# Performance work log

Measured on AMD Instinct MI355X. Metric: run time of the kernel, lower is better.

## Reference

```python
import jax, jax.numpy as jnp
import numpy as np

B, T, C, H = 256, 256, 384, 64  # batch, seq (= block_size), n_embd, head_size


def setup_inputs() -> dict:
    key = jax.random.key(0)
    kx, kq, kk, kv = jax.random.split(key, 4)
    x = jax.random.normal(kx, (B, T, C), dtype=jnp.float32)
    # nn.Linear(n_embd, head_size, bias=False) weights, stored transposed so y = x @ W
    scale = 1.0 / np.sqrt(C)
    Wq = jax.random.normal(kq, (C, H), dtype=jnp.float32) * scale
    Wk = jax.random.normal(kk, (C, H), dtype=jnp.float32) * scale
    Wv = jax.random.normal(kv, (C, H), dtype=jnp.float32) * scale
    return {"x": x, "Wq": Wq, "Wk": Wk, "Wv": Wv}


def reference(x, Wq, Wk, Wv):
    # Single causal self-attention head. NOTE: source scales by C**-0.5 where
    # C = n_embd (not head_size) — preserved faithfully. Dropout in eval mode
    # (identity) for a deterministic reference.
    Bv, Tv, Cv = x.shape
    q = x @ Wq                                   # [B, T, H]
    k = x @ Wk                                   # [B, T, H]
    v = x @ Wv                                   # [B, T, H]
    wei = jnp.einsum('bth,bsh->bts', q, k) * (Cv ** -0.5)  # [B, T, T]
    causal = jnp.tril(jnp.ones((Tv, Tv), dtype=bool))      # tril[:T,:T]
    wei = jnp.where(causal[None, :, :], wei, -jnp.inf)
    wei = jax.nn.softmax(wei, axis=-1)
    out = jnp.einsum('bts,bsh->bth', wei, v)     # [B, T, H]
    return out
```

## Files before the change

### kernel.cpp

```cpp
#include <hip/hip_runtime.h>
#include <hip/hip_bf16.h>

typedef __attribute__((ext_vector_type(8))) short bf16x8;
typedef __attribute__((ext_vector_type(4))) float f32x4;

__device__ __forceinline__ unsigned short f2bf(float f) {
    union { float f; unsigned int u; } v; v.f = f;
    unsigned int u = v.u;
    unsigned int r = u + 0x7FFFu + ((u >> 16) & 1u);
    return (unsigned short)(r >> 16);
}

__device__ __forceinline__ unsigned int cvtpk(float lo, float hi) {
    unsigned int r;
    asm("v_cvt_pk_bf16_f32 %0, %1, %2" : "=v"(r) : "v"(lo), "v"(hi));
    return r;
}

#define GLDS16(gsrc, ldst)                                                          \
    __builtin_amdgcn_global_load_lds(                                               \
        (const __attribute__((address_space(1))) unsigned int*)(gsrc),              \
        (__attribute__((address_space(3))) unsigned int*)(ldst), 16, 0, 0)

__global__ __launch_bounds__(256) void wprep(const float* __restrict__ Wq,
                                             const float* __restrict__ Wk,
                                             const float* __restrict__ Wv,
                                             unsigned short* __restrict__ Wt2) {
    int idx = blockIdx.x * 256 + threadIdx.x;
    if (idx >= 73728) return;
    int w   = idx / 24576;
    int rem = idx % 24576;
    int n = rem / 384, k = rem % 384;
    const float* W = (w == 0) ? Wq : ((w == 1) ? Wk : Wv);
    int col = w * 64 + n;
    Wt2[(size_t)(k >> 5) * 6144 + ((k >> 3) & 3) * 1536 + col * 8 + (k & 7)] = f2bf(W[k * 64 + n]);
}

#define QOFF  0
#define KOFF  36864
#define VTOFF 73728
#define POFF  107520

__global__ __launch_bounds__(512, 2) void fused(const float* __restrict__ x,
                                                const unsigned short* __restrict__ Wt2,
                                                float* __restrict__ out) {
    __shared__ __align__(16) char smem[147456];

    const int b = blockIdx.x;
    const int tid = threadIdx.x, lane = tid & 63, wid = tid >> 6;
    const int l15 = lane & 15, lg = lane >> 4;
    const float* xb = x + (size_t)b * 98304;
    float* ob = out + (size_t)b * 16384;

#pragma unroll
    for (int i = 0; i < 18; ++i) {
        int n = wid * 18 + i;
        GLDS16(Wt2 + (size_t)n * 512 + lane * 8, smem + n * 1024);
    }

    const float* xw = xb + (size_t)(wid * 32 + l15) * 384 + lg * 8;

    float4 p0[4], p1[4], p2[4];
#define XLOAD(P, C)                                                                 \
    P[0] = *reinterpret_cast<const float4*>(xw + (C) * 32);                         \
    P[1] = *reinterpret_cast<const float4*>(xw + (C) * 32 + 4);                     \
    P[2] = *reinterpret_cast<const float4*>(xw + 6144 + (C) * 32);                  \
    P[3] = *reinterpret_cast<const float4*>(xw + 6144 + (C) * 32 + 4);
    XLOAD(p0, 0)
    XLOAD(p1, 1)
    XLOAD(p2, 2)
    __builtin_amdgcn_sched_barrier(0);
    asm volatile("s_waitcnt vmcnt(12)" ::: "memory");
    __builtin_amdgcn_s_barrier();

    f32x4 acc[2][12] = {};

#define CHUNK(C, P, WAITN)                                                          \
    asm volatile("s_waitcnt vmcnt(" #WAITN ")" ::: "memory");                       \
    __builtin_amdgcn_sched_barrier(0);                                              \
    {                                                                               \
        union { unsigned int u[4]; bf16x8 v; } cv0, cv1;                            \
        cv0.u[0] = cvtpk(P[0].x, P[0].y); cv0.u[1] = cvtpk(P[0].z, P[0].w);         \
        cv0.u[2] = cvtpk(P[1].x, P[1].y); cv0.u[3] = cvtpk(P[1].z, P[1].w);         \
        cv1.u[0] = cvtpk(P[2].x, P[2].y); cv1.u[1] = cvtpk(P[2].z, P[2].w);         \
        cv1.u[2] = cvtpk(P[3].x, P[3].y); cv1.u[3] = cvtpk(P[3].z, P[3].w);         \
        bf16x8 a0 = cv0.v, a1 = cv1.v;                                              \
        if ((C) + 3 < 12) { XLOAD(P, (C) + 3) }                                     \
        __builtin_amdgcn_sched_barrier(0);                                          \
        const char* bs = smem + (C) * 12288 + lg * 3072 + l15 * 16;                 \
        _Pragma("unroll")                                                           \
        for (int n = 0; n < 12; ++n) {                                              \
            bf16x8 bf = *reinterpret_cast<const bf16x8*>(bs + n * 256);             \
            acc[0][n] = __builtin_amdgcn_mfma_f32_16x16x32_bf16(a0, bf, acc[0][n], 0, 0, 0); \
            acc[1][n] = __builtin_amdgcn_mfma_f32_16x16x32_bf16(a1, bf, acc[1][n], 0, 0, 0); \
        }                                                                           \
    }

    CHUNK(0,  p0, 8)
    CHUNK(1,  p1, 8)
    CHUNK(2,  p2, 8)
    CHUNK(3,  p0, 8)
    CHUNK(4,  p1, 8)
    CHUNK(5,  p2, 8)
    CHUNK(6,  p0, 8)
    CHUNK(7,  p1, 8)
    CHUNK(8,  p2, 8)
    CHUNK(9,  p0, 8)
    CHUNK(10, p1, 4)
    CHUNK(11, p2, 0)

    __syncthreads();

#pragma unroll
    for (int m = 0; m < 2; ++m) {
#pragma unroll
        for (int n = 0; n < 12; ++n) {
            int col = n * 16 + l15;
#pragma unroll
            for (int j = 0; j < 4; ++j) {
                int t = wid * 32 + m * 16 + lg * 4 + j;
                unsigned short hv = f2bf(acc[m][n][j]);
                if (col < 64)
                    *reinterpret_cast<unsigned short*>(smem + QOFF + (t * 72 + col) * 2) = hv;
                else if (col < 128)
                    *reinterpret_cast<unsigned short*>(smem + KOFF + (t * 72 + (col - 64)) * 2) = hv;
                else
                    *reinterpret_cast<unsigned short*>(smem + VTOFF + ((col - 128) * 264 + t) * 2) = hv;
            }
        }
    }
    __syncthreads();

    char* Pw = smem + POFF + wid * 4608;
    const int r0 = wid * 32;
    const float scale = 0.05103103630798287f;

    f32x4 o[2][4] = {};
    float M[2][4], L[2][4];
#pragma unroll
    for (int m = 0; m < 2; ++m)
#pragma unroll
        for (int j = 0; j < 4; ++j) { M[m][j] = -1e30f; L[m][j] = 0.f; }

    for (int jt = 0; jt <= (wid >> 1); ++jt) {
        f32x4 s[2][4] = {};
#pragma unroll
        for (int kk = 0; kk < 2; ++kk) {
            bf16x8 aq[2], bk[4];
#pragma unroll
            for (int m = 0; m < 2; ++m)
                aq[m] = *reinterpret_cast<const bf16x8*>(smem + QOFF + ((r0 + m * 16 + l15) * 72 + kk * 32 + lg * 8) * 2);
#pragma unroll
            for (int n = 0; n < 4; ++n)
                bk[n] = *reinterpret_cast<const bf16x8*>(smem + KOFF + ((jt * 64 + n * 16 + l15) * 72 + kk * 32 + lg * 8) * 2);
#pragma unroll
            for (int m = 0; m < 2; ++m)
#pragma unroll
                for (int n = 0; n < 4; ++n)
                    s[m][n] = __builtin_amdgcn_mfma_f32_16x16x32_bf16(aq[m], bk[n], s[m][n], 0, 0, 0);
        }
        float tm[2][4];
#pragma unroll
        for (int m = 0; m < 2; ++m)
#pragma unroll
            for (int j = 0; j < 4; ++j) tm[m][j] = -1e30f;
#pragma unroll
        for (int m = 0; m < 2; ++m) {
#pragma unroll
            for (int n = 0; n < 4; ++n) {
                int colg = jt * 64 + n * 16 + l15;
#pragma unroll
                for (int j = 0; j < 4; ++j) {
                    int rowg = r0 + m * 16 + lg * 4 + j;
                    float v = s[m][n][j] * scale;
                    if (colg > rowg) v = -1e30f;
                    s[m][n][j] = v;
                    tm[m][j] = fmaxf(tm[m][j], v);
                }
            }
        }
#pragma unroll
        for (int m = 0; m < 2; ++m)
#pragma unroll
            for (int j = 0; j < 4; ++j) {
                float v = tm[m][j];
                v = fmaxf(v, __shfl_xor(v, 1));
                v = fmaxf(v, __shfl_xor(v, 2));
                v = fmaxf(v, __shfl_xor(v, 4));
                v = fmaxf(v, __shfl_xor(v, 8));
                tm[m][j] = v;
            }
        float alpha[2][4];
#pragma unroll
        for (int m = 0; m < 2; ++m)
#pragma unroll
            for (int j = 0; j < 4; ++j) {
                float mn = fmaxf(M[m][j], tm[m][j]);
                alpha[m][j] = __expf(M[m][j] - mn);
                M[m][j] = mn;
            }
        float ts[2][4] = {};
#pragma unroll
        for (int m = 0; m < 2; ++m)
#pragma unroll
            for (int n = 0; n < 4; ++n)
#pragma unroll
                for (int j = 0; j < 4; ++j) {
                    float p = __expf(s[m][n][j] - M[m][j]);
                    s[m][n][j] = p;
                    ts[m][j] += p;
                }
#pragma unroll
        for (int m = 0; m < 2; ++m)
#pragma unroll
            for (int j = 0; j < 4; ++j) {
                float v = ts[m][j];
                v += __shfl_xor(v, 1);
                v += __shfl_xor(v, 2);
                v += __shfl_xor(v, 4);
                v += __shfl_xor(v, 8);
                L[m][j] = L[m][j] * alpha[m][j] + v;
            }
#pragma unroll
        for (int m = 0; m < 2; ++m)
#pragma unroll
            for (int n = 0; n < 4; ++n)
#pragma unroll
                for (int j = 0; j < 4; ++j) o[m][n][j] *= alpha[m][j];
#pragma unroll
        for (int m = 0; m < 2; ++m)
#pragma unroll
            for (int n = 0; n < 4; ++n)
#pragma unroll
                for (int j = 0; j < 4; ++j)
                    *reinterpret_cast<unsigned short*>(Pw + ((m * 16 + lg * 4 + j) * 72 + n * 16 + l15) * 2) = f2bf(s[m][n][j]);
        asm volatile("s_waitcnt lgkmcnt(0)" ::: "memory");
#pragma unroll
        for (int kk = 0; kk < 2; ++kk) {
            bf16x8 ap[2], bv[4];
#pragma unroll
            for (int m = 0; m < 2; ++m)
                ap[m] = *reinterpret_cast<const bf16x8*>(Pw + ((m * 16 + l15) * 72 + kk * 32 + lg * 8) * 2);
#pragma unroll
            for (int n = 0; n < 4; ++n)
                bv[n] = *reinterpret_cast<const bf16x8*>(smem + VTOFF + ((n * 16 + l15) * 264 + jt * 64 + kk * 32 + lg * 8) * 2);
#pragma unroll
            for (int m = 0; m < 2; ++m)
#pragma unroll
                for (int n = 0; n < 4; ++n)
                    o[m][n] = __builtin_amdgcn_mfma_f32_16x16x32_bf16(ap[m], bv[n], o[m][n], 0, 0, 0);
        }
    }
#pragma unroll
    for (int m = 0; m < 2; ++m) {
#pragma unroll
        for (int n = 0; n < 4; ++n) {
            int h = n * 16 + l15;
#pragma unroll
            for (int j = 0; j < 4; ++j) {
                int t = r0 + m * 16 + lg * 4 + j;
                ob[(size_t)t * 64 + h] = o[m][n][j] / L[m][j];
            }
        }
    }
}

extern "C" void kernel_launch(void* const* d_in, const int* in_sizes, int n_in,
                              void* d_out, int out_size, void* d_ws, size_t ws_size,
                              hipStream_t stream) {
    const float* x  = (const float*)d_in[0];
    const float* Wq = (const float*)d_in[1];
    const float* Wk = (const float*)d_in[2];
    const float* Wv = (const float*)d_in[3];
    float* out = (float*)d_out;

    unsigned short* Wt2 = (unsigned short*)d_ws;

    wprep<<<288, 256, 0, stream>>>(Wq, Wk, Wv, Wt2);
    fused<<<256, 512, 0, stream>>>(x, Wt2, out);
}
```

Baseline: 41.09 us.

## Use 1024-thread blocks with 16 rows per wave instead of 32

Doubles the workgroup to 16 waves and halves each wave's share: 16 token rows in both the QKV projection and the causal attention, instead of 32. This removes the two-row-tile register arrays and spreads the triangular attention work over more waves, aiming for more latency hiding and better per-wave balance. In exchange, each K/V LDS fragment is now reused by only one MFMA row tile instead of two, so LDS traffic per FLOP goes up. The old launch bound of 2 blocks per CU is dropped.

```diff
diff --git a/kernel.cpp b/kernel.cpp
--- a/kernel.cpp
+++ b/kernel.cpp
@@ -41,9 +41,9 @@
 #define VTOFF 73728
 #define POFF  107520
 
-__global__ __launch_bounds__(512, 2) void fused(const float* __restrict__ x,
-                                                const unsigned short* __restrict__ Wt2,
-                                                float* __restrict__ out) {
+__global__ __launch_bounds__(1024) void fused(const float* __restrict__ x,
+                                              const unsigned short* __restrict__ Wt2,
+                                              float* __restrict__ out) {
     __shared__ __align__(16) char smem[147456];
 
     const int b = blockIdx.x;
@@ -53,214 +53,176 @@
     float* ob = out + (size_t)b * 16384;
 
 #pragma unroll
-    for (int i = 0; i < 18; ++i) {
-        int n = wid * 18 + i;
+    for (int i = 0; i < 9; ++i) {
+        int n = wid * 9 + i;
         GLDS16(Wt2 + (size_t)n * 512 + lane * 8, smem + n * 1024);
     }
 
-    const float* xw = xb + (size_t)(wid * 32 + l15) * 384 + lg * 8;
-
-    float4 p0[4], p1[4], p2[4];
+    const float* xw = xb + (size_t)(wid * 16 + l15) * 384 + lg * 8;
+
+    float4 p0[2], p1[2], p2[2];
 #define XLOAD(P, C)                                                                 \
     P[0] = *reinterpret_cast<const float4*>(xw + (C) * 32);                         \
-    P[1] = *reinterpret_cast<const float4*>(xw + (C) * 32 + 4);                     \
-    P[2] = *reinterpret_cast<const float4*>(xw + 6144 + (C) * 32);                  \
-    P[3] = *reinterpret_cast<const float4*>(xw + 6144 + (C) * 32 + 4);
+    P[1] = *reinterpret_cast<const float4*>(xw + (C) * 32 + 4);
     XLOAD(p0, 0)
     XLOAD(p1, 1)
     XLOAD(p2, 2)
     __builtin_amdgcn_sched_barrier(0);
-    asm volatile("s_waitcnt vmcnt(12)" ::: "memory");
+    asm volatile("s_waitcnt vmcnt(6)" ::: "memory");
     __builtin_amdgcn_s_barrier();
 
-    f32x4 acc[2][12] = {};
+    f32x4 acc[12] = {};
 
 #define CHUNK(C, P, WAITN)                                                          \
     asm volatile("s_waitcnt vmcnt(" #WAITN ")" ::: "memory");                       \
     __builtin_amdgcn_sched_barrier(0);                                              \
     {                                                                               \
-        union { unsigned int u[4]; bf16x8 v; } cv0, cv1;                            \
+        union { unsigned int u[4]; bf16x8 v; } cv0;                                 \
         cv0.u[0] = cvtpk(P[0].x, P[0].y); cv0.u[1] = cvtpk(P[0].z, P[0].w);         \
         cv0.u[2] = cvtpk(P[1].x, P[1].y); cv0.u[3] = cvtpk(P[1].z, P[1].w);         \
-        cv1.u[0] = cvtpk(P[2].x, P[2].y); cv1.u[1] = cvtpk(P[2].z, P[2].w);         \
-        cv1.u[2] = cvtpk(P[3].x, P[3].y); cv1.u[3] = cvtpk(P[3].z, P[3].w);         \
-        bf16x8 a0 = cv0.v, a1 = cv1.v;                                              \
+        bf16x8 a0 = cv0.v;                                                          \
         if ((C) + 3 < 12) { XLOAD(P, (C) + 3) }                                     \
         __builtin_amdgcn_sched_barrier(0);                                          \
         const char* bs = smem + (C) * 12288 + lg * 3072 + l15 * 16;                 \
         _Pragma("unroll")                                                           \
         for (int n = 0; n < 12; ++n) {                                              \
             bf16x8 bf = *reinterpret_cast<const bf16x8*>(bs + n * 256);             \
-            acc[0][n] = __builtin_amdgcn_mfma_f32_16x16x32_bf16(a0, bf, acc[0][n], 0, 0, 0); \
-            acc[1][n] = __builtin_amdgcn_mfma_f32_16x16x32_bf16(a1, bf, acc[1][n], 0, 0, 0); \
+            acc[n] = __builtin_amdgcn_mfma_f32_16x16x32_bf16(a0, bf, acc[n], 0, 0, 0); \
         }                                                                           \
     }
 
-    CHUNK(0,  p0, 8)
-    CHUNK(1,  p1, 8)
-    CHUNK(2,  p2, 8)
-    CHUNK(3,  p0, 8)
-    CHUNK(4,  p1, 8)
-    CHUNK(5,  p2, 8)
-    CHUNK(6,  p0, 8)
-    CHUNK(7,  p1, 8)
-    CHUNK(8,  p2, 8)
-    CHUNK(9,  p0, 8)
-    CHUNK(10, p1, 4)
+    CHUNK(0,  p0, 4)
+    CHUNK(1,  p1, 4)
+    CHUNK(2,  p2, 4)
+    CHUNK(3,  p0, 4)
+    CHUNK(4,  p1, 4)
+    CHUNK(5,  p2, 4)
+    CHUNK(6,  p0, 4)
+    CHUNK(7,  p1, 4)
+    CHUNK(8,  p2, 4)
+    CHUNK(9,  p0, 4)
+    CHUNK(10, p1, 2)
     CHUNK(11, p2, 0)
 
     __syncthreads();
 
 #pragma unroll
-    for (int m = 0; m < 2; ++m) {
-#pragma unroll
-        for (int n = 0; n < 12; ++n) {
-            int col = n * 16 + l15;
+    for (int n = 0; n < 12; ++n) {
+        int col = n * 16 + l15;
+#pragma unroll
+        for (int j = 0; j < 4; ++j) {
+            int t = wid * 16 + lg * 4 + j;
+            unsigned short hv = f2bf(acc[n][j]);
+            if (col < 64)
+                *reinterpret_cast<unsigned short*>(smem + QOFF + (t * 72 + col) * 2) = hv;
+            else if (col < 128)
+                *reinterpret_cast<unsigned short*>(smem + KOFF + (t * 72 + (col - 64)) * 2) = hv;
+            else
+                *reinterpret_cast<unsigned short*>(smem + VTOFF + ((col - 128) * 264 + t) * 2) = hv;
+        }
+    }
+    __syncthreads();
+
+    char* Pw = smem + POFF + wid * 2304;
+    const int r0 = wid * 16;
+    const float scale = 0.05103103630798287f;
+
+    f32x4 o[4] = {};
+    float M[4], L[4];
+#pragma unroll
+    for (int j = 0; j < 4; ++j) { M[j] = -1e30f; L[j] = 0.f; }
+
+    for (int jt = 0; jt <= (wid >> 2); ++jt) {
+        f32x4 s[4] = {};
+#pragma unroll
+        for (int kk = 0; kk < 2; ++kk) {
+            bf16x8 aq, bk[4];
+            aq = *reinterpret_cast<const bf16x8*>(smem + QOFF + ((r0 + l15) * 72 + kk * 32 + lg * 8) * 2);
+#pragma unroll
+            for (int n = 0; n < 4; ++n)
+                bk[n] = *reinterpret_cast<const bf16x8*>(smem + KOFF + ((jt * 64 + n * 16 + l15) * 72 + kk * 32 + lg * 8) * 2);
+#pragma unroll
+            for (int n = 0; n < 4; ++n)
+                s[n] = __builtin_amdgcn_mfma_f32_16x16x32_bf16(aq, bk[n], s[n], 0, 0, 0);
+        }
+        float tm[4];
+#pragma unroll
+        for (int j = 0; j < 4; ++j) tm[j] = -1e30f;
+#pragma unroll
+        for (int n = 0; n < 4; ++n) {
+            int colg = jt * 64 + n * 16 + l15;
 #pragma unroll
             for (int j = 0; j < 4; ++j) {
-                int t = wid * 32 + m * 16 + lg * 4 + j;
-                unsigned short hv = f2bf(acc[m][n][j]);
-                if (col < 64)
-                    *reinterpret_cast<unsigned short*>(smem + QOFF + (t * 72 + col) * 2) = hv;
-                else if (col < 128)
-                    *reinterpret_cast<unsigned short*>(smem + KOFF + (t * 72 + (col - 64)) * 2) = hv;
-                else
-                    *reinterpret_cast<unsigned short*>(smem + VTOFF + ((col - 128) * 264 + t) * 2) = hv;
+                int rowg = r0 + lg * 4 + j;
+                float v = s[n][j] * scale;
+                if (colg > rowg) v = -1e30f;
+                s[n][j] = v;
+                tm[j] = fmaxf(tm[j], v);
             }
         }
-    }
-    __syncthreads();
-
-    char* Pw = smem + POFF + wid * 4608;
-    const int r0 = wid * 32;
-    const float scale = 0.05103103630798287f;
-
-    f32x4 o[2][4] = {};
-    float M[2][4], L[2][4];
-#pragma unroll
-    for (int m = 0; m < 2; ++m)
-#pragma unroll
-        for (int j = 0; j < 4; ++j) { M[m][j] = -1e30f; L[m][j] = 0.f; }
-
-    for (int jt = 0; jt <= (wid >> 1); ++jt) {
-        f32x4 s[2][4] = {};
+#pragma unroll
+        for (int j = 0; j < 4; ++j) {
+            float v = tm[j];
+            v = fmaxf(v, __shfl_xor(v, 1));
+            v = fmaxf(v, __shfl_xor(v, 2));
+            v = fmaxf(v, __shfl_xor(v, 4));
+            v = fmaxf(v, __shfl_xor(v, 8));
+            tm[j] = v;
+        }
+        float alpha[4];
+#pragma unroll
+        for (int j = 0; j < 4; ++j) {
+            float mn = fmaxf(M[j], tm[j]);
+            alpha[j] = __expf(M[j] - mn);
+            M[j] = mn;
+        }
+        float ts[4] = {};
+#pragma unroll
+        for (int n = 0; n < 4; ++n)
+#pragma unroll
+            for (int j = 0; j < 4; ++j) {
+                float p = __expf(s[n][j] - M[j]);
+                s[n][j] = p;
+                ts[j] += p;
+            }
+#pragma unroll
+        for (int j = 0; j < 4; ++j) {
+            float v = ts[j];
+            v += __shfl_xor(v, 1);
+            v += __shfl_xor(v, 2);
+            v += __shfl_xor(v, 4);
+            v += __shfl_xor(v, 8);
+            L[j] = L[j] * alpha[j] + v;
+        }
+#pragma unroll
+        for (int n = 0; n < 4; ++n)
+#pragma unroll
+            for (int j = 0; j < 4; ++j) o[n][j] *= alpha[j];
+#pragma unroll
+        for (int n = 0; n < 4; ++n)
+#pragma unroll
+            for (int j = 0; j < 4; ++j)
+                *reinterpret_cast<unsigned short*>(Pw + ((lg * 4 + j) * 72 + n * 16 + l15) * 2) = f2bf(s[n][j]);
+        asm volatile("s_waitcnt lgkmcnt(0)" ::: "memory");
 #pragma unroll
         for (int kk = 0; kk < 2; ++kk) {
-            bf16x8 aq[2], bk[4];
-#pragma unroll
-            for (int m = 0; m < 2; ++m)
-                aq[m] = *reinterpret_cast<const bf16x8*>(smem + QOFF + ((r0 + m * 16 + l15) * 72 + kk * 32 + lg * 8) * 2);
-#pragma unroll
-            for (int n = 0; n < 4; ++n)
-                bk[n] = *reinterpret_cast<const bf16x8*>(smem + KOFF + ((jt * 64 + n * 16 + l15) * 72 + kk * 32 + lg * 8) * 2);
-#pragma unroll
-            for (int m = 0; m < 2; ++m)
-#pragma unroll
-                for (int n = 0; n < 4; ++n)
-                    s[m][n] = __builtin_amdgcn_mfma_f32_16x16x32_bf16(aq[m], bk[n], s[m][n], 0, 0, 0);
-        }
-        float tm[2][4];
-#pragma unroll
-        for (int m = 0; m < 2; ++m)
-#pragma unroll
-            for (int j = 0; j < 4; ++j) tm[m][j] = -1e30f;
-#pragma unroll
-        for (int m = 0; m < 2; ++m) {
-#pragma unroll
-            for (int n = 0; n < 4; ++n) {
-                int colg = jt * 64 + n * 16 + l15;
-#pragma unroll
-                for (int j = 0; j < 4; ++j) {
-                    int rowg = r0 + m * 16 + lg * 4 + j;
-                    float v = s[m][n][j] * scale;
-                    if (colg > rowg) v = -1e30f;
-                    s[m][n][j] = v;
-                    tm[m][j] = fmaxf(tm[m][j], v);
-                }
-            }
-        }
-#pragma unroll
-        for (int m = 0; m < 2; ++m)
-#pragma unroll
-            for (int j = 0; j < 4; ++j) {
-                float v = tm[m][j];
-                v = fmaxf(v, __shfl_xor(v, 1));
-                v = fmaxf(v, __shfl_xor(v, 2));
-                v = fmaxf(v, __shfl_xor(v, 4));
-                v = fmaxf(v, __shfl_xor(v, 8));
-                tm[m][j] = v;
-            }
-        float alpha[2][4];
-#pragma unroll
-        for (int m = 0; m < 2; ++m)
-#pragma unroll
-            for (int j = 0; j < 4; ++j) {
-                float mn = fmaxf(M[m][j], tm[m][j]);
-                alpha[m][j] = __expf(M[m][j] - mn);
-                M[m][j] = mn;
-            }
-        float ts[2][4] = {};
-#pragma unroll
-        for (int m = 0; m < 2; ++m)
-#pragma unroll
-            for (int n = 0; n < 4; ++n)
-#pragma unroll
-                for (int j = 0; j < 4; ++j) {
-                    float p = __expf(s[m][n][j] - M[m][j]);
-                    s[m][n][j] = p;
-                    ts[m][j] += p;
-                }
-#pragma unroll
-        for (int m = 0; m < 2; ++m)
-#pragma unroll
-            for (int j = 0; j < 4; ++j) {
-                float v = ts[m][j];
-                v += __shfl_xor(v, 1);
-                v += __shfl_xor(v, 2);
-                v += __shfl_xor(v, 4);
-                v += __shfl_xor(v, 8);
-                L[m][j] = L[m][j] * alpha[m][j] + v;
-            }
-#pragma unroll
-        for (int m = 0; m < 2; ++m)
-#pragma unroll
-            for (int n = 0; n < 4; ++n)
-#pragma unroll
-                for (int j = 0; j < 4; ++j) o[m][n][j] *= alpha[m][j];
-#pragma unroll
-        for (int m = 0; m < 2; ++m)
-#pragma unroll
-            for (int n = 0; n < 4; ++n)
-#pragma unroll
-                for (int j = 0; j < 4; ++j)
-                    *reinterpret_cast<unsigned short*>(Pw + ((m * 16 + lg * 4 + j) * 72 + n * 16 + l15) * 2) = f2bf(s[m][n][j]);
-        asm volatile("s_waitcnt lgkmcnt(0)" ::: "memory");
-#pragma unroll
-        for (int kk = 0; kk < 2; ++kk) {
-            bf16x8 ap[2], bv[4];
-#pragma unroll
-            for (int m = 0; m < 2; ++m)
-                ap[m] = *reinterpret_cast<const bf16x8*>(Pw + ((m * 16 + l15) * 72 + kk * 32 + lg * 8) * 2);
+            bf16x8 ap, bv[4];
+            ap = *reinterpret_cast<const bf16x8*>(Pw + (l15 * 72 + kk * 32 + lg * 8) * 2);
 #pragma unroll
             for (int n = 0; n < 4; ++n)
                 bv[n] = *reinterpret_cast<const bf16x8*>(smem + VTOFF + ((n * 16 + l15) * 264 + jt * 64 + kk * 32 + lg * 8) * 2);
 #pragma unroll
-            for (int m = 0; m < 2; ++m)
-#pragma unroll
-                for (int n = 0; n < 4; ++n)
-                    o[m][n] = __builtin_amdgcn_mfma_f32_16x16x32_bf16(ap[m], bv[n], o[m][n], 0, 0, 0);
-        }
-    }
-#pragma unroll
-    for (int m = 0; m < 2; ++m) {
-#pragma unroll
-        for (int n = 0; n < 4; ++n) {
-            int h = n * 16 + l15;
-#pragma unroll
-            for (int j = 0; j < 4; ++j) {
-                int t = r0 + m * 16 + lg * 4 + j;
-                ob[(size_t)t * 64 + h] = o[m][n][j] / L[m][j];
-            }
+            for (int n = 0; n < 4; ++n)
+                o[n] = __builtin_amdgcn_mfma_f32_16x16x32_bf16(ap, bv[n], o[n], 0, 0, 0);
+        }
+    }
+#pragma unroll
+    for (int n = 0; n < 4; ++n) {
+        int h = n * 16 + l15;
+#pragma unroll
+        for (int j = 0; j < 4; ++j) {
+            int t = r0 + lg * 4 + j;
+            ob[(size_t)t * 64 + h] = o[n][j] / L[j];
         }
     }
 }
@@ -277,5 +239,5 @@
     unsigned short* Wt2 = (unsigned short*)d_ws;
 
     wprep<<<288, 256, 0, stream>>>(Wq, Wk, Wv, Wt2);
-    fused<<<256, 512, 0, stream>>>(x, Wt2, out);
-}
+    fused<<<256, 1024, 0, stream>>>(x, Wt2, out);
+}
```

Result: faster. 39.89 us (-2.9%).

## Use single-pass softmax with templated tile counts and deepen x prefetch

Applied to the files above, without the earlier changes.

Replaces the online-softmax loop with a templated per-warp routine that computes all score tiles into registers first. It then takes one max, one exp/sum pass and the PV product, which removes the per-tile rescaling and the runtime loop. The x load pipeline is deepened from 3 to 5 chunks in flight. Launch bounds drop to 1 block per CU so the larger register footprint fits. Occupancy was already limited by the 144KB of shared memory, but the higher register pressure and the extra code size from four template instantiations are the risks.

```diff
diff --git a/kernel.cpp b/kernel.cpp
--- a/kernel.cpp
+++ b/kernel.cpp
@@ -41,7 +41,131 @@
 #define VTOFF 73728
 #define POFF  107520
 
-__global__ __launch_bounds__(512, 2) void fused(const float* __restrict__ x,
+template<int NT>
+__device__ __forceinline__ void attn_strip(char* smem, char* Pw, float* ob,
+                                           int r0, int l15, int lg) {
+    const float scale = 0.05103103630798287f;
+
+    bf16x8 aq[2][2];
+#pragma unroll
+    for (int m = 0; m < 2; ++m)
+#pragma unroll
+        for (int kk = 0; kk < 2; ++kk)
+            aq[m][kk] = *reinterpret_cast<const bf16x8*>(smem + QOFF + ((r0 + m * 16 + l15) * 72 + kk * 32 + lg * 8) * 2);
+
+    f32x4 s[NT][2][4] = {};
+#pragma unroll
+    for (int jt = 0; jt < NT; ++jt) {
+#pragma unroll
+        for (int kk = 0; kk < 2; ++kk) {
+            bf16x8 bk[4];
+#pragma unroll
+            for (int n = 0; n < 4; ++n)
+                bk[n] = *reinterpret_cast<const bf16x8*>(smem + KOFF + ((jt * 64 + n * 16 + l15) * 72 + kk * 32 + lg * 8) * 2);
+#pragma unroll
+            for (int m = 0; m < 2; ++m)
+#pragma unroll
+                for (int n = 0; n < 4; ++n)
+                    s[jt][m][n] = __builtin_amdgcn_mfma_f32_16x16x32_bf16(aq[m][kk], bk[n], s[jt][m][n], 0, 0, 0);
+        }
+    }
+    float M[2][4];
+#pragma unroll
+    for (int m = 0; m < 2; ++m)
+#pragma unroll
+        for (int j = 0; j < 4; ++j) M[m][j] = -1e30f;
+#pragma unroll
+    for (int jt = 0; jt < NT; ++jt)
+#pragma unroll
+        for (int m = 0; m < 2; ++m)
+#pragma unroll
+            for (int n = 0; n < 4; ++n) {
+                int colg = jt * 64 + n * 16 + l15;
+#pragma unroll
+                for (int j = 0; j < 4; ++j) {
+                    int rowg = r0 + m * 16 + lg * 4 + j;
+                    float v = s[jt][m][n][j] * scale;
+                    if (colg > rowg) v = -1e30f;
+                    s[jt][m][n][j] = v;
+                    M[m][j] = fmaxf(M[m][j], v);
+                }
+            }
+#pragma unroll
+    for (int m = 0; m < 2; ++m)
+#pragma unroll
+        for (int j = 0; j < 4; ++j) {
+            float v = M[m][j];
+            v = fmaxf(v, __shfl_xor(v, 1));
+            v = fmaxf(v, __shfl_xor(v, 2));
+            v = fmaxf(v, __shfl_xor(v, 4));
+            v = fmaxf(v, __shfl_xor(v, 8));
+            M[m][j] = v;
+        }
+    float L[2][4] = {};
+#pragma unroll
+    for (int jt = 0; jt < NT; ++jt)
+#pragma unroll
+        for (int m = 0; m < 2; ++m)
+#pragma unroll
+            for (int n = 0; n < 4; ++n)
+#pragma unroll
+                for (int j = 0; j < 4; ++j) {
+                    float p = __expf(s[jt][m][n][j] - M[m][j]);
+                    s[jt][m][n][j] = p;
+                    L[m][j] += p;
+                }
+#pragma unroll
+    for (int m = 0; m < 2; ++m)
+#pragma unroll
+        for (int j = 0; j < 4; ++j) {
+            float v = L[m][j];
+            v += __shfl_xor(v, 1);
+            v += __shfl_xor(v, 2);
+            v += __shfl_xor(v, 4);
+            v += __shfl_xor(v, 8);
+            L[m][j] = v;
+        }
+    f32x4 o[2][4] = {};
+#pragma unroll
+    for (int jt = 0; jt < NT; ++jt) {
+#pragma unroll
+        for (int m = 0; m < 2; ++m)
+#pragma unroll
+            for (int n = 0; n < 4; ++n)
+#pragma unroll
+                for (int j = 0; j < 4; ++j)
+                    *reinterpret_cast<unsigned short*>(Pw + ((m * 16 + lg * 4 + j) * 72 + n * 16 + l15) * 2) = f2bf(s[jt][m][n][j]);
+        asm volatile("s_waitcnt lgkmcnt(0)" ::: "memory");
+#pragma unroll
+        for (int kk = 0; kk < 2; ++kk) {
+            bf16x8 ap[2], bv[4];
+#pragma unroll
+            for (int m = 0; m < 2; ++m)
+                ap[m] = *reinterpret_cast<const bf16x8*>(Pw + ((m * 16 + l15) * 72 + kk * 32 + lg * 8) * 2);
+#pragma unroll
+            for (int n = 0; n < 4; ++n)
+                bv[n] = *reinterpret_cast<const bf16x8*>(smem + VTOFF + ((n * 16 + l15) * 264 + jt * 64 + kk * 32 + lg * 8) * 2);
+#pragma unroll
+            for (int m = 0; m < 2; ++m)
+#pragma unroll
+                for (int n = 0; n < 4; ++n)
+                    o[m][n] = __builtin_amdgcn_mfma_f32_16x16x32_bf16(ap[m], bv[n], o[m][n], 0, 0, 0);
+        }
+    }
+#pragma unroll
+    for (int m = 0; m < 2; ++m)
+#pragma unroll
+        for (int n = 0; n < 4; ++n) {
+            int h = n * 16 + l15;
+#pragma unroll
+            for (int j = 0; j < 4; ++j) {
+                int t = r0 + m * 16 + lg * 4 + j;
+                ob[(size_t)t * 64 + h] = o[m][n][j] / L[m][j];
+            }
+        }
+}
+
+__global__ __launch_bounds__(512, 1) void fused(const float* __restrict__ x,
                                                 const unsigned short* __restrict__ Wt2,
                                                 float* __restrict__ out) {
     __shared__ __align__(16) char smem[147456];
@@ -60,7 +184,7 @@
 
     const float* xw = xb + (size_t)(wid * 32 + l15) * 384 + lg * 8;
 
-    float4 p0[4], p1[4], p2[4];
+    float4 p0[4], p1[4], p2[4], p3[4], p4[4];
 #define XLOAD(P, C)                                                                 \
     P[0] = *reinterpret_cast<const float4*>(xw + (C) * 32);                         \
     P[1] = *reinterpret_cast<const float4*>(xw + (C) * 32 + 4);                     \
@@ -69,8 +193,10 @@
     XLOAD(p0, 0)
     XLOAD(p1, 1)
     XLOAD(p2, 2)
+    XLOAD(p3, 3)
+    XLOAD(p4, 4)
     __builtin_amdgcn_sched_barrier(0);
-    asm volatile("s_waitcnt vmcnt(12)" ::: "memory");
+    asm volatile("s_waitcnt vmcnt(20)" ::: "memory");
     __builtin_amdgcn_s_barrier();
 
     f32x4 acc[2][12] = {};
@@ -85,7 +211,7 @@
         cv1.u[0] = cvtpk(P[2].x, P[2].y); cv1.u[1] = cvtpk(P[2].z, P[2].w);         \
         cv1.u[2] = cvtpk(P[3].x, P[3].y); cv1.u[3] = cvtpk(P[3].z, P[3].w);         \
         bf16x8 a0 = cv0.v, a1 = cv1.v;                                              \
-        if ((C) + 3 < 12) { XLOAD(P, (C) + 3) }                                     \
+        if ((C) + 5 < 12) { XLOAD(P, (C) + 5) }                                     \
         __builtin_amdgcn_sched_barrier(0);                                          \
         const char* bs = smem + (C) * 12288 + lg * 3072 + l15 * 16;                 \
         _Pragma("unroll")                                                           \
@@ -96,18 +222,18 @@
         }                                                                           \
     }
 
-    CHUNK(0,  p0, 8)
-    CHUNK(1,  p1, 8)
-    CHUNK(2,  p2, 8)
-    CHUNK(3,  p0, 8)
-    CHUNK(4,  p1, 8)
-    CHUNK(5,  p2, 8)
-    CHUNK(6,  p0, 8)
-    CHUNK(7,  p1, 8)
-    CHUNK(8,  p2, 8)
-    CHUNK(9,  p0, 8)
-    CHUNK(10, p1, 4)
-    CHUNK(11, p2, 0)
+    CHUNK(0,  p0, 16)
+    CHUNK(1,  p1, 16)
+    CHUNK(2,  p2, 16)
+    CHUNK(3,  p3, 16)
+    CHUNK(4,  p4, 16)
+    CHUNK(5,  p0, 16)
+    CHUNK(6,  p1, 16)
+    CHUNK(7,  p2, 16)
+    CHUNK(8,  p3, 12)
+    CHUNK(9,  p4, 8)
+    CHUNK(10, p0, 4)
+    CHUNK(11, p1, 0)
 
     __syncthreads();
 
@@ -133,136 +259,10 @@
 
     char* Pw = smem + POFF + wid * 4608;
     const int r0 = wid * 32;
-    const float scale = 0.05103103630798287f;
-
-    f32x4 o[2][4] = {};
-    float M[2][4], L[2][4];
-#pragma unroll
-    for (int m = 0; m < 2; ++m)
-#pragma unroll
-        for (int j = 0; j < 4; ++j) { M[m][j] = -1e30f; L[m][j] = 0.f; }
-
-    for (int jt = 0; jt <= (wid >> 1); ++jt) {
-        f32x4 s[2][4] = {};
-#pragma unroll
-        for (int kk = 0; kk < 2; ++kk) {
-            bf16x8 aq[2], bk[4];
-#pragma unroll
-            for (int m = 0; m < 2; ++m)
-                aq[m] = *reinterpret_cast<const bf16x8*>(smem + QOFF + ((r0 + m * 16 + l15) * 72 + kk * 32 + lg * 8) * 2);
-#pragma unroll
-            for (int n = 0; n < 4; ++n)
-                bk[n] = *reinterpret_cast<const bf16x8*>(smem + KOFF + ((jt * 64 + n * 16 + l15) * 72 + kk * 32 + lg * 8) * 2);
-#pragma unroll
-            for (int m = 0; m < 2; ++m)
-#pragma unroll
-                for (int n = 0; n < 4; ++n)
-                    s[m][n] = __builtin_amdgcn_mfma_f32_16x16x32_bf16(aq[m], bk[n], s[m][n], 0, 0, 0);
-        }
-        float tm[2][4];
-#pragma unroll
-        for (int m = 0; m < 2; ++m)
-#pragma unroll
-            for (int j = 0; j < 4; ++j) tm[m][j] = -1e30f;
-#pragma unroll
-        for (int m = 0; m < 2; ++m) {
-#pragma unroll
-            for (int n = 0; n < 4; ++n) {
-                int colg = jt * 64 + n * 16 + l15;
-#pragma unroll
-                for (int j = 0; j < 4; ++j) {
-                    int rowg = r0 + m * 16 + lg * 4 + j;
-                    float v = s[m][n][j] * scale;
-                    if (colg > rowg) v = -1e30f;
-                    s[m][n][j] = v;
-                    tm[m][j] = fmaxf(tm[m][j], v);
-                }
-            }
-        }
-#pragma unroll
-        for (int m = 0; m < 2; ++m)
-#pragma unroll
-            for (int j = 0; j < 4; ++j) {
-                float v = tm[m][j];
-                v = fmaxf(v, __shfl_xor(v, 1));
-                v = fmaxf(v, __shfl_xor(v, 2));
-                v = fmaxf(v, __shfl_xor(v, 4));
-                v = fmaxf(v, __shfl_xor(v, 8));
-                tm[m][j] = v;
-            }
-        float alpha[2][4];
-#pragma unroll
-        for (int m = 0; m < 2; ++m)
-#pragma unroll
-            for (int j = 0; j < 4; ++j) {
-                float mn = fmaxf(M[m][j], tm[m][j]);
-                alpha[m][j] = __expf(M[m][j] - mn);
-                M[m][j] = mn;
-            }
-        float ts[2][4] = {};
-#pragma unroll
-        for (int m = 0; m < 2; ++m)
-#pragma unroll
-            for (int n = 0; n < 4; ++n)
-#pragma unroll
-                for (int j = 0; j < 4; ++j) {
-                    float p = __expf(s[m][n][j] - M[m][j]);
-                    s[m][n][j] = p;
-                    ts[m][j] += p;
-                }
-#pragma unroll
-        for (int m = 0; m < 2; ++m)
-#pragma unroll
-            for (int j = 0; j < 4; ++j) {
-                float v = ts[m][j];
-                v += __shfl_xor(v, 1);
-                v += __shfl_xor(v, 2);
-                v += __shfl_xor(v, 4);
-                v += __shfl_xor(v, 8);
-                L[m][j] = L[m][j] * alpha[m][j] + v;
-            }
-#pragma unroll
-        for (int m = 0; m < 2; ++m)
-#pragma unroll
-            for (int n = 0; n < 4; ++n)
-#pragma unroll
-                for (int j = 0; j < 4; ++j) o[m][n][j] *= alpha[m][j];
-#pragma unroll
-        for (int m = 0; m < 2; ++m)
-#pragma unroll
-            for (int n = 0; n < 4; ++n)
-#pragma unroll
-                for (int j = 0; j < 4; ++j)
-                    *reinterpret_cast<unsigned short*>(Pw + ((m * 16 + lg * 4 + j) * 72 + n * 16 + l15) * 2) = f2bf(s[m][n][j]);
-        asm volatile("s_waitcnt lgkmcnt(0)" ::: "memory");
-#pragma unroll
-        for (int kk = 0; kk < 2; ++kk) {
-            bf16x8 ap[2], bv[4];
-#pragma unroll
-            for (int m = 0; m < 2; ++m)
-                ap[m] = *reinterpret_cast<const bf16x8*>(Pw + ((m * 16 + l15) * 72 + kk * 32 + lg * 8) * 2);
-#pragma unroll
-            for (int n = 0; n < 4; ++n)
-                bv[n] = *reinterpret_cast<const bf16x8*>(smem + VTOFF + ((n * 16 + l15) * 264 + jt * 64 + kk * 32 + lg * 8) * 2);
-#pragma unroll
-            for (int m = 0; m < 2; ++m)
-#pragma unroll
-                for (int n = 0; n < 4; ++n)
-                    o[m][n] = __builtin_amdgcn_mfma_f32_16x16x32_bf16(ap[m], bv[n], o[m][n], 0, 0, 0);
-        }
-    }
-#pragma unroll
-    for (int m = 0; m < 2; ++m) {
-#pragma unroll
-        for (int n = 0; n < 4; ++n) {
-            int h = n * 16 + l15;
-#pragma unroll
-            for (int j = 0; j < 4; ++j) {
-                int t = r0 + m * 16 + lg * 4 + j;
-                ob[(size_t)t * 64 + h] = o[m][n][j] / L[m][j];
-            }
-        }
-    }
+    if (wid < 2)      attn_strip<1>(smem, Pw, ob, r0, l15, lg);
+    else if (wid < 4) attn_strip<2>(smem, Pw, ob, r0, l15, lg);
+    else if (wid < 6) attn_strip<3>(smem, Pw, ob, r0, l15, lg);
+    else              attn_strip<4>(smem, Pw, ob, r0, l15, lg);
 }
 
 extern "C" void kernel_launch(void* const* d_in, const int* in_sizes, int n_in,
```

Measured after the change: 39.49 us. 3.9% less time.
